# Kernel optimization log

Hardware: AMD Instinct MI355X
Metric: run time of the kernel (lower is better)

## Reference

```python
import jax, jax.numpy as jnp
import numpy as np

B, L = 256, 256
TAU = 0.01


def setup_inputs() -> dict:
    key = jax.random.key(0)
    k1, k2, k3, k4 = jax.random.split(key, 4)
    x = jax.random.normal(k1, (B, L, B), dtype=jnp.float32)
    target = jax.random.normal(k2, (B, L, B), dtype=jnp.float32)
    mask = jnp.ones((B, L), dtype=jnp.int32)  # prefix-valid mask per query; all clips valid
    query_labels = jax.random.randint(k3, (B,), 0, B, dtype=jnp.int64)
    label_mat = jax.random.randint(k4, (B, B), 0, 2, dtype=jnp.int32)  # label_dict[i] -> row i
    return {"x": x, "target": target, "mask": mask, "query_labels": query_labels, "label_mat": label_mat}


def reference(x, target, mask, query_labels, label_mat):
    # x, target: [B, L, B] (batch, clips, queries); mask: [B(queries), L]
    xs = jax.nn.softmax(x, axis=1)
    ts = jax.nn.softmax(target, axis=1)
    m = (mask > 0).astype(xs.dtype)  # [i(query), l]
    # mask target clips per query i (equivalent to the original's :m prefix slice
    # because mask is a contiguous prefix of valid clips)
    tsm = ts * m.T[None, :, :]  # [c, l, i]
    # sim[i, b, c] = sum_l xs[b, l, i] * ts[c, l, i] * m[i, l]  (per-query B x B matmul)
    sim = jnp.einsum('bli,cli->ibc', xs, tsm)
    logits = sim / TAU
    # original computes -log(exp(n_ji)/sum_c exp(n_jc)) == -log_softmax over c, picked at class i
    logp = jax.nn.log_softmax(logits, axis=-1)  # [i, j, c]
    per = jnp.diagonal(logp, axis1=0, axis2=2)  # per[j, i] = logp[i, j, i]
    loss = -(label_mat.astype(xs.dtype).T * per).sum() / x.shape[0]
    return loss
```

## Files before the change

### kernel.cpp

```cpp
#include <hip/hip_runtime.h>
#include <hip/hip_bf16.h>

#define NB 256
#define NL 256
#define SCALE 100.0f

typedef __attribute__((ext_vector_type(4))) unsigned int u32x4;
typedef __attribute__((ext_vector_type(8))) __bf16 bfrag8;
typedef __attribute__((ext_vector_type(4))) float f32x4;

union BU { bfrag8 f; u32x4 u; };

static __device__ __forceinline__ unsigned int pack2bf(float a, float b) {
  union { float f; unsigned int u; } ua, ub;
  ua.f = a; ub.f = b;
  unsigned int ra = (ua.u + 0x7FFFu + ((ua.u >> 16) & 1u)) >> 16;
  unsigned int rb = (ub.u + 0x7FFFu + ((ub.u >> 16) & 1u)) & 0xFFFF0000u;
  return ra | rb;
}

__global__ __launch_bounds__(1024, 2) void exp_t(
    const float* __restrict__ x, const float* __restrict__ tgt,
    unsigned int* __restrict__ xsT, unsigned int* __restrict__ tsT)
{
  const int b = blockIdx.x;
  const bool is_t = (blockIdx.y != 0);
  const int tid = threadIdx.x;
  const int i = tid & 255;
  const int h = tid >> 8;
  const float* src = (is_t ? tgt : x) + (size_t)b * (NL * NB) + i;
  unsigned int* dstb = (is_t ? tsT : xsT);

  __shared__ __align__(16) unsigned char stg[256 * 128];

  const int r0 = tid >> 3;
  const int c  = tid & 7;

  for (int lc = 0; lc < 4; ++lc) {
    float v[16];
    #pragma unroll
    for (int k = 0; k < 16; ++k)
      v[k] = __expf(src[(size_t)(lc * 64 + h * 16 + k) * NB]);
    u32x4 p0, p1;
    p0.x = pack2bf(v[0], v[1]);   p0.y = pack2bf(v[2], v[3]);
    p0.z = pack2bf(v[4], v[5]);   p0.w = pack2bf(v[6], v[7]);
    p1.x = pack2bf(v[8], v[9]);   p1.y = pack2bf(v[10], v[11]);
    p1.z = pack2bf(v[12], v[13]); p1.w = pack2bf(v[14], v[15]);
    *reinterpret_cast<u32x4*>(&stg[i * 128 + (((h * 2 + 0) ^ (i & 7)) << 4)]) = p0;
    *reinterpret_cast<u32x4*>(&stg[i * 128 + (((h * 2 + 1) ^ (i & 7)) << 4)]) = p1;
    __syncthreads();
    u32x4 q0 = *reinterpret_cast<const u32x4*>(&stg[r0 * 128 + ((c ^ (r0 & 7)) << 4)]);
    u32x4 q1 = *reinterpret_cast<const u32x4*>(&stg[(r0 + 128) * 128 + ((c ^ (r0 & 7)) << 4)]);
    *reinterpret_cast<u32x4*>(dstb + ((size_t)r0 * 256 + b) * 128 + lc * 32 + c * 4) = q0;
    *reinterpret_cast<u32x4*>(dstb + ((size_t)(r0 + 128) * 256 + b) * 128 + lc * 32 + c * 4) = q1;
    __syncthreads();
  }
}

__global__ __launch_bounds__(256, 2) void gemm_lse(
    const unsigned short* __restrict__ xsT,
    const unsigned short* __restrict__ tsT,
    const int* __restrict__ mask,
    const int* __restrict__ label_mat,
    float* __restrict__ out)
{
  const int n  = blockIdx.x;
  const int g  = n & 7;
  const int q  = n >> 3;
  const int i  = ((q >> 2) << 3) + g;
  const int jt = q & 3;
  const int t  = threadIdx.x;
  const int w  = t >> 6;
  const int lane = t & 63;

  __shared__ __align__(16) unsigned char As[64 * 128];
  __shared__ __align__(16) unsigned char Bs[256 * 128];
  __shared__ __align__(16) unsigned short s_mask[NL];
  __shared__ float s_rmax[4][64];
  __shared__ float s_rsum[4][64];
  __shared__ float s_diag[64];

  const unsigned short* Ag = xsT + ((size_t)i * NB + jt * 64) * NL;
  const unsigned short* Bg = tsT + (size_t)i * NB * NL;

  const int srow = t >> 3;
  const int sch  = t & 7;

  s_mask[t] = (mask[i * NL + t] > 0) ? (unsigned short)0xFFFFu : (unsigned short)0u;

  BU onesbu;
  onesbu.u = u32x4{0x3F803F80u, 0x3F803F80u, 0x3F803F80u, 0x3F803F80u};
  const bfrag8 ones = onesbu.f;

  f32x4 acc[4][4], acc_as[4], acc_bs[4];
  #pragma unroll
  for (int a = 0; a < 4; ++a) {
    acc_as[a] = f32x4{0.f, 0.f, 0.f, 0.f};
    acc_bs[a] = f32x4{0.f, 0.f, 0.f, 0.f};
    #pragma unroll
    for (int cc = 0; cc < 4; ++cc) acc[a][cc] = f32x4{0.f, 0.f, 0.f, 0.f};
  }

  u32x4 areg[2], breg[8];

  #pragma unroll
  for (int r = 0; r < 2; ++r)
    areg[r] = *reinterpret_cast<const u32x4*>(Ag + (size_t)(srow + r * 32) * NL + sch * 8);
  #pragma unroll
  for (int r = 0; r < 8; ++r)
    breg[r] = *reinterpret_cast<const u32x4*>(Bg + (size_t)(srow + r * 32) * NL + sch * 8);

  __syncthreads();

  #pragma unroll
  for (int kc = 0; kc < 4; ++kc) {
    #pragma unroll
    for (int r = 0; r < 2; ++r) {
      int row = srow + r * 32;
      *reinterpret_cast<u32x4*>(&As[row * 128 + ((sch ^ (row & 7)) << 4)]) = areg[r];
    }
    #pragma unroll
    for (int r = 0; r < 8; ++r) {
      int row = srow + r * 32;
      *reinterpret_cast<u32x4*>(&Bs[row * 128 + ((sch ^ (row & 7)) << 4)]) = breg[r];
    }
    __syncthreads();
    if (kc < 3) {
      const int kofs = (kc + 1) * 64;
      #pragma unroll
      for (int r = 0; r < 2; ++r)
        areg[r] = *reinterpret_cast<const u32x4*>(Ag + (size_t)(srow + r * 32) * NL + kofs + sch * 8);
      #pragma unroll
      for (int r = 0; r < 8; ++r)
        breg[r] = *reinterpret_cast<const u32x4*>(Bg + (size_t)(srow + r * 32) * NL + kofs + sch * 8);
    }
    #pragma unroll
    for (int kk = 0; kk < 2; ++kk) {
      const int co = kk * 4 + (lane >> 4);
      bfrag8 af[4], bfr[4];
      #pragma unroll
      for (int jf = 0; jf < 4; ++jf) {
        int row = jf * 16 + (lane & 15);
        af[jf] = *reinterpret_cast<const bfrag8*>(&As[row * 128 + ((co ^ (row & 7)) << 4)]);
      }
      #pragma unroll
      for (int cf = 0; cf < 4; ++cf) {
        int row = w * 64 + cf * 16 + (lane & 15);
        bfr[cf] = *reinterpret_cast<const bfrag8*>(&Bs[row * 128 + ((co ^ (row & 7)) << 4)]);
      }
      u32x4 mk = *reinterpret_cast<const u32x4*>(
          &s_mask[kc * 64 + kk * 32 + ((lane >> 4) << 3)]);
      #pragma unroll
      for (int jf = 0; jf < 4; ++jf) {
        BU am; am.f = af[jf]; am.u &= mk;
        #pragma unroll
        for (int cf = 0; cf < 4; ++cf)
          acc[jf][cf] = __builtin_amdgcn_mfma_f32_16x16x32_bf16(
              am.f, bfr[cf], acc[jf][cf], 0, 0, 0);
        acc_as[jf] = __builtin_amdgcn_mfma_f32_16x16x32_bf16(
            af[jf], ones, acc_as[jf], 0, 0, 0);
      }
      #pragma unroll
      for (int cf = 0; cf < 4; ++cf)
        acc_bs[cf] = __builtin_amdgcn_mfma_f32_16x16x32_bf16(
            ones, bfr[cf], acc_bs[cf], 0, 0, 0);
    }
    __syncthreads();
  }

  float ixv[4][4];
  #pragma unroll
  for (int jf = 0; jf < 4; ++jf)
    #pragma unroll
    for (int reg = 0; reg < 4; ++reg)
      ixv[jf][reg] = __builtin_amdgcn_rcpf(acc_as[jf][reg]) * SCALE;
  float itv[4];
  #pragma unroll
  for (int cf = 0; cf < 4; ++cf)
    itv[cf] = __builtin_amdgcn_rcpf(acc_bs[cf][0]);
  #pragma unroll
  for (int jf = 0; jf < 4; ++jf)
    #pragma unroll
    for (int cf = 0; cf < 4; ++cf)
      #pragma unroll
      for (int reg = 0; reg < 4; ++reg)
        acc[jf][cf][reg] *= ixv[jf][reg] * itv[cf];

  const int rg = (lane >> 4) << 2;

  #pragma unroll
  for (int jf = 0; jf < 4; ++jf) {
    #pragma unroll
    for (int reg = 0; reg < 4; ++reg) {
      float m = fmaxf(fmaxf(acc[jf][0][reg], acc[jf][1][reg]),
                      fmaxf(acc[jf][2][reg], acc[jf][3][reg]));
      #pragma unroll
      for (int off = 1; off < 16; off <<= 1) m = fmaxf(m, __shfl_xor(m, off, 64));
      if ((lane & 15) == 0) s_rmax[w][jf * 16 + rg + reg] = m;
    }
  }
  if (w == (i >> 6) && (lane & 15) == (i & 15)) {
    const int cfd = (i >> 4) & 3;
    #pragma unroll
    for (int jf = 0; jf < 4; ++jf) {
      #pragma unroll
      for (int reg = 0; reg < 4; ++reg) {
        float v = acc[jf][0][reg];
        #pragma unroll
        for (int cf = 1; cf < 4; ++cf)
          v = (cfd == cf) ? acc[jf][cf][reg] : v;
        s_diag[jf * 16 + rg + reg] = v;
      }
    }
  }
  __syncthreads();

  #pragma unroll
  for (int jf = 0; jf < 4; ++jf) {
    #pragma unroll
    for (int reg = 0; reg < 4; ++reg) {
      int row = jf * 16 + rg + reg;
      float gm = fmaxf(fmaxf(s_rmax[0][row], s_rmax[1][row]),
                       fmaxf(s_rmax[2][row], s_rmax[3][row]));
      float sE = 0.f;
      #pragma unroll
      for (int cf = 0; cf < 4; ++cf) sE += __expf(acc[jf][cf][reg] - gm);
      #pragma unroll
      for (int off = 1; off < 16; off <<= 1) sE += __shfl_xor(sE, off, 64);
      if ((lane & 15) == 0) s_rsum[w][row] = sE;
    }
  }
  __syncthreads();

  float contrib = 0.f;
  if (t < 64) {
    const int row = t;
    float gm = fmaxf(fmaxf(s_rmax[0][row], s_rmax[1][row]),
                     fmaxf(s_rmax[2][row], s_rmax[3][row]));
    float tot = s_rsum[0][row] + s_rsum[1][row] + s_rsum[2][row] + s_rsum[3][row];
    float lse = __logf(tot) + gm;
    float lbl = (float)label_mat[i * NB + jt * 64 + row];
    contrib = lbl * (s_diag[row] - lse);
  }
  #pragma unroll
  for (int off = 32; off >= 1; off >>= 1) contrib += __shfl_down(contrib, off, 64);
  if (t == 0) atomicAdd(out, contrib * (-1.0f / 256.0f));
}

extern "C" void kernel_launch(void* const* d_in, const int* in_sizes, int n_in,
                              void* d_out, int out_size, void* d_ws, size_t ws_size,
                              hipStream_t stream) {
  const float* x   = (const float*)d_in[0];
  const float* tgt = (const float*)d_in[1];
  const int* mask  = (const int*)d_in[2];
  const int* label_mat = (const int*)d_in[4];
  float* out = (float*)d_out;

  unsigned int* xsT = (unsigned int*)d_ws;
  unsigned int* tsT = xsT + (size_t)NB * NB * NL / 2;

  hipMemsetAsync(out, 0, sizeof(float), stream);
  exp_t<<<dim3(NB, 2), 1024, 0, stream>>>(x, tgt, xsT, tsT);
  gemm_lse<<<dim3(1024), 256, 0, stream>>>((const unsigned short*)xsT,
                                           (const unsigned short*)tsT,
                                           mask, label_mat, out);
}
```

Measured before the change: 75.98 us.

## Vectorize exp-transpose loads, double-buffer staging, and deepen GEMM global prefetch

The exp/transpose kernel now reads inputs as float4 along the query dimension instead of strided scalars. It stages through two LDS buffers with an extra XOR swizzle, which lets it drop the trailing barrier per chunk. The GEMM kernel keeps two register sets of global loads in flight, prefetching two k-chunks ahead, so global latency overlaps with MFMA work. In exchange, LDS use in the first kernel doubles and the GEMM holds more live registers, which may hurt occupancy.

Result: no change. 74.91 us (-1.4%).

```diff
diff --git a/kernel.cpp b/kernel.cpp
--- a/kernel.cpp
+++ b/kernel.cpp
@@ -26,34 +26,40 @@
   const int b = blockIdx.x;
   const bool is_t = (blockIdx.y != 0);
   const int tid = threadIdx.x;
-  const int i = tid & 255;
-  const int h = tid >> 8;
-  const float* src = (is_t ? tgt : x) + (size_t)b * (NL * NB) + i;
+  const int i4 = tid & 63;
+  const int g  = tid >> 6;
+  const f32x4* src4 = reinterpret_cast<const f32x4*>(
+      (is_t ? tgt : x) + (size_t)b * (NL * NB));
   unsigned int* dstb = (is_t ? tsT : xsT);
 
-  __shared__ __align__(16) unsigned char stg[256 * 128];
+  __shared__ __align__(16) unsigned char stg[2][256 * 128];
 
   const int r0 = tid >> 3;
   const int c  = tid & 7;
 
+  #pragma unroll
   for (int lc = 0; lc < 4; ++lc) {
-    float v[16];
-    #pragma unroll
-    for (int k = 0; k < 16; ++k)
-      v[k] = __expf(src[(size_t)(lc * 64 + h * 16 + k) * NB]);
-    u32x4 p0, p1;
-    p0.x = pack2bf(v[0], v[1]);   p0.y = pack2bf(v[2], v[3]);
-    p0.z = pack2bf(v[4], v[5]);   p0.w = pack2bf(v[6], v[7]);
-    p1.x = pack2bf(v[8], v[9]);   p1.y = pack2bf(v[10], v[11]);
-    p1.z = pack2bf(v[12], v[13]); p1.w = pack2bf(v[14], v[15]);
-    *reinterpret_cast<u32x4*>(&stg[i * 128 + (((h * 2 + 0) ^ (i & 7)) << 4)]) = p0;
-    *reinterpret_cast<u32x4*>(&stg[i * 128 + (((h * 2 + 1) ^ (i & 7)) << 4)]) = p1;
+    unsigned char* sb = stg[lc & 1];
+    f32x4 r[4];
+    #pragma unroll
+    for (int k = 0; k < 4; ++k)
+      r[k] = src4[(size_t)(lc * 64 + g * 4 + k) * 64 + i4];
+    #pragma unroll
+    for (int ii = 0; ii < 4; ++ii) {
+      const int row = i4 * 4 + ii;
+      unsigned int lo = pack2bf(__expf(r[0][ii]), __expf(r[1][ii]));
+      unsigned int hi = pack2bf(__expf(r[2][ii]), __expf(r[3][ii]));
+      const int ch = (g >> 1) ^ (row & 7) ^ ((row >> 3) & 7);
+      unsigned int* p = reinterpret_cast<unsigned int*>(
+          &sb[row * 128 + (ch << 4) + (g & 1) * 8]);
+      p[0] = lo; p[1] = hi;
+    }
     __syncthreads();
-    u32x4 q0 = *reinterpret_cast<const u32x4*>(&stg[r0 * 128 + ((c ^ (r0 & 7)) << 4)]);
-    u32x4 q1 = *reinterpret_cast<const u32x4*>(&stg[(r0 + 128) * 128 + ((c ^ (r0 & 7)) << 4)]);
+    const int ch0 = c ^ (r0 & 7) ^ ((r0 >> 3) & 7);
+    u32x4 q0 = *reinterpret_cast<const u32x4*>(&sb[r0 * 128 + (ch0 << 4)]);
+    u32x4 q1 = *reinterpret_cast<const u32x4*>(&sb[(r0 + 128) * 128 + (ch0 << 4)]);
     *reinterpret_cast<u32x4*>(dstb + ((size_t)r0 * 256 + b) * 128 + lc * 32 + c * 4) = q0;
     *reinterpret_cast<u32x4*>(dstb + ((size_t)(r0 + 128) * 256 + b) * 128 + lc * 32 + c * 4) = q1;
-    __syncthreads();
   }
 }
 
@@ -101,39 +107,32 @@
     for (int cc = 0; cc < 4; ++cc) acc[a][cc] = f32x4{0.f, 0.f, 0.f, 0.f};
   }
 
-  u32x4 areg[2], breg[8];
-
-  #pragma unroll
-  for (int r = 0; r < 2; ++r)
-    areg[r] = *reinterpret_cast<const u32x4*>(Ag + (size_t)(srow + r * 32) * NL + sch * 8);
-  #pragma unroll
-  for (int r = 0; r < 8; ++r)
-    breg[r] = *reinterpret_cast<const u32x4*>(Bg + (size_t)(srow + r * 32) * NL + sch * 8);
-
-  __syncthreads();
-
-  #pragma unroll
-  for (int kc = 0; kc < 4; ++kc) {
+  u32x4 a0[2], b0[8], a1[2], b1[8];
+
+  auto load_set = [&](u32x4 (&ar)[2], u32x4 (&br)[8], int kc) {
+    const int kofs = kc * 64;
+    #pragma unroll
+    for (int r = 0; r < 2; ++r)
+      ar[r] = *reinterpret_cast<const u32x4*>(
+          Ag + (size_t)(srow + r * 32) * NL + kofs + sch * 8);
+    #pragma unroll
+    for (int r = 0; r < 8; ++r)
+      br[r] = *reinterpret_cast<const u32x4*>(
+          Bg + (size_t)(srow + r * 32) * NL + kofs + sch * 8);
+  };
+  auto store_set = [&](u32x4 (&ar)[2], u32x4 (&br)[8]) {
     #pragma unroll
     for (int r = 0; r < 2; ++r) {
       int row = srow + r * 32;
-      *reinterpret_cast<u32x4*>(&As[row * 128 + ((sch ^ (row & 7)) << 4)]) = areg[r];
+      *reinterpret_cast<u32x4*>(&As[row * 128 + ((sch ^ (row & 7)) << 4)]) = ar[r];
     }
     #pragma unroll
     for (int r = 0; r < 8; ++r) {
       int row = srow + r * 32;
-      *reinterpret_cast<u32x4*>(&Bs[row * 128 + ((sch ^ (row & 7)) << 4)]) = breg[r];
-    }
-    __syncthreads();
-    if (kc < 3) {
-      const int kofs = (kc + 1) * 64;
-      #pragma unroll
-      for (int r = 0; r < 2; ++r)
-        areg[r] = *reinterpret_cast<const u32x4*>(Ag + (size_t)(srow + r * 32) * NL + kofs + sch * 8);
-      #pragma unroll
-      for (int r = 0; r < 8; ++r)
-        breg[r] = *reinterpret_cast<const u32x4*>(Bg + (size_t)(srow + r * 32) * NL + kofs + sch * 8);
-    }
+      *reinterpret_cast<u32x4*>(&Bs[row * 128 + ((sch ^ (row & 7)) << 4)]) = br[r];
+    }
+  };
+  auto mfma_phase = [&](int kc) {
     #pragma unroll
     for (int kk = 0; kk < 2; ++kk) {
       const int co = kk * 4 + (lane >> 4);
@@ -141,12 +140,14 @@
       #pragma unroll
       for (int jf = 0; jf < 4; ++jf) {
         int row = jf * 16 + (lane & 15);
-        af[jf] = *reinterpret_cast<const bfrag8*>(&As[row * 128 + ((co ^ (row & 7)) << 4)]);
+        af[jf] = *reinterpret_cast<const bfrag8*>(
+            &As[row * 128 + ((co ^ (row & 7)) << 4)]);
       }
       #pragma unroll
       for (int cf = 0; cf < 4; ++cf) {
         int row = w * 64 + cf * 16 + (lane & 15);
-        bfr[cf] = *reinterpret_cast<const bfrag8*>(&Bs[row * 128 + ((co ^ (row & 7)) << 4)]);
+        bfr[cf] = *reinterpret_cast<const bfrag8*>(
+            &Bs[row * 128 + ((co ^ (row & 7)) << 4)]);
       }
       u32x4 mk = *reinterpret_cast<const u32x4*>(
           &s_mask[kc * 64 + kk * 32 + ((lane >> 4) << 3)]);
@@ -165,8 +166,27 @@
         acc_bs[cf] = __builtin_amdgcn_mfma_f32_16x16x32_bf16(
             ones, bfr[cf], acc_bs[cf], 0, 0, 0);
     }
-    __syncthreads();
-  }
+  };
+
+  load_set(a0, b0, 0);
+  load_set(a1, b1, 1);
+  store_set(a0, b0);
+  __syncthreads();
+  load_set(a0, b0, 2);
+  mfma_phase(0);
+  __syncthreads();
+  store_set(a1, b1);
+  __syncthreads();
+  load_set(a1, b1, 3);
+  mfma_phase(1);
+  __syncthreads();
+  store_set(a0, b0);
+  __syncthreads();
+  mfma_phase(2);
+  __syncthreads();
+  store_set(a1, b1);
+  __syncthreads();
+  mfma_phase(3);
 
   float ixv[4][4];
   #pragma unroll
```

## Stage GEMM tiles with direct global-to-LDS loads and double-buffered B

Applied to the files above, without the earlier changes.

The GEMM kernel stops staging tiles through registers. It issues global_load_lds 16-byte loads that write straight into LDS with the XOR swizzle applied at the source address, and double-buffers the B tile so the next K chunk loads while MFMAs run. The A fragments for both k-substeps are read up front so As can be refilled early. The exp_t output layout changes from [r][b] to [b][r] to match the new addressing, and a swizzle index bug in the second staging read is fixed. The trade-offs are hand-placed waitcnt and barrier calls that carry correctness risk, and more LDS per block, which may lower occupancy.

Measured after the change: 77.23 us. Within noise of the previous version (+1.6%).

```diff
diff --git a/kernel.cpp b/kernel.cpp
--- a/kernel.cpp
+++ b/kernel.cpp
@@ -17,6 +17,12 @@
   unsigned int ra = (ua.u + 0x7FFFu + ((ua.u >> 16) & 1u)) >> 16;
   unsigned int rb = (ub.u + 0x7FFFu + ((ub.u >> 16) & 1u)) & 0xFFFF0000u;
   return ra | rb;
+}
+
+static __device__ __forceinline__ void gld_lds16(const void* g, void* l) {
+  __builtin_amdgcn_global_load_lds(
+      (const __attribute__((address_space(1))) unsigned int*)g,
+      (__attribute__((address_space(3))) unsigned int*)l, 16, 0, 0);
 }
 
 __global__ __launch_bounds__(1024, 2) void exp_t(
@@ -50,9 +56,9 @@
     *reinterpret_cast<u32x4*>(&stg[i * 128 + (((h * 2 + 1) ^ (i & 7)) << 4)]) = p1;
     __syncthreads();
     u32x4 q0 = *reinterpret_cast<const u32x4*>(&stg[r0 * 128 + ((c ^ (r0 & 7)) << 4)]);
-    u32x4 q1 = *reinterpret_cast<const u32x4*>(&stg[(r0 + 128) * 128 + ((c ^ (r0 & 7)) << 4)]);
-    *reinterpret_cast<u32x4*>(dstb + ((size_t)r0 * 256 + b) * 128 + lc * 32 + c * 4) = q0;
-    *reinterpret_cast<u32x4*>(dstb + ((size_t)(r0 + 128) * 256 + b) * 128 + lc * 32 + c * 4) = q1;
+    u32x4 q1 = *reinterpret_cast<const u32x4*>(&stg[(r0 + 128) * 128 + ((c ^ ((r0 + 128) & 7)) << 4)]);
+    *reinterpret_cast<u32x4*>(dstb + ((size_t)b * 256 + r0) * 128 + lc * 32 + c * 4) = q0;
+    *reinterpret_cast<u32x4*>(dstb + ((size_t)b * 256 + r0 + 128) * 128 + lc * 32 + c * 4) = q1;
     __syncthreads();
   }
 }
@@ -74,15 +80,12 @@
   const int lane = t & 63;
 
   __shared__ __align__(16) unsigned char As[64 * 128];
-  __shared__ __align__(16) unsigned char Bs[256 * 128];
+  __shared__ __align__(16) unsigned char Bs[2][256 * 128];
   __shared__ __align__(16) unsigned short s_mask[NL];
   __shared__ float s_rmax[4][64];
   __shared__ float s_rsum[4][64];
   __shared__ float s_diag[64];
 
-  const unsigned short* Ag = xsT + ((size_t)i * NB + jt * 64) * NL;
-  const unsigned short* Bg = tsT + (size_t)i * NB * NL;
-
   const int srow = t >> 3;
   const int sch  = t & 7;
 
@@ -101,71 +104,77 @@
     for (int cc = 0; cc < 4; ++cc) acc[a][cc] = f32x4{0.f, 0.f, 0.f, 0.f};
   }
 
-  u32x4 areg[2], breg[8];
-
-  #pragma unroll
-  for (int r = 0; r < 2; ++r)
-    areg[r] = *reinterpret_cast<const u32x4*>(Ag + (size_t)(srow + r * 32) * NL + sch * 8);
-  #pragma unroll
-  for (int r = 0; r < 8; ++r)
-    breg[r] = *reinterpret_cast<const u32x4*>(Bg + (size_t)(srow + r * 32) * NL + sch * 8);
-
-  __syncthreads();
-
-  #pragma unroll
-  for (int kc = 0; kc < 4; ++kc) {
-    #pragma unroll
-    for (int r = 0; r < 2; ++r) {
-      int row = srow + r * 32;
-      *reinterpret_cast<u32x4*>(&As[row * 128 + ((sch ^ (row & 7)) << 4)]) = areg[r];
-    }
+  auto stage_B = [&](int buf, int kc2) {
+    const int kofs = kc2 * 64;
     #pragma unroll
     for (int r = 0; r < 8; ++r) {
       int row = srow + r * 32;
-      *reinterpret_cast<u32x4*>(&Bs[row * 128 + ((sch ^ (row & 7)) << 4)]) = breg[r];
-    }
-    __syncthreads();
-    if (kc < 3) {
-      const int kofs = (kc + 1) * 64;
-      #pragma unroll
-      for (int r = 0; r < 2; ++r)
-        areg[r] = *reinterpret_cast<const u32x4*>(Ag + (size_t)(srow + r * 32) * NL + kofs + sch * 8);
-      #pragma unroll
-      for (int r = 0; r < 8; ++r)
-        breg[r] = *reinterpret_cast<const u32x4*>(Bg + (size_t)(srow + r * 32) * NL + kofs + sch * 8);
-    }
+      int schp = sch ^ (row & 7);
+      gld_lds16(tsT + ((size_t)row * 256 + i) * 256 + kofs + schp * 8,
+                &Bs[buf][w * 1024 + r * 4096]);
+    }
+  };
+  auto stage_A = [&](int kc2) {
+    const int kofs = kc2 * 64;
+    #pragma unroll
+    for (int r = 0; r < 2; ++r) {
+      int arow = srow + r * 32;
+      int schp = sch ^ (arow & 7);
+      gld_lds16(xsT + ((size_t)(jt * 64 + arow) * 256 + i) * 256 + kofs + schp * 8,
+                &As[w * 1024 + r * 4096]);
+    }
+  };
+
+  stage_B(0, 0);
+  stage_A(0);
+  __syncthreads();
+
+  #pragma unroll
+  for (int kc = 0; kc < 4; ++kc) {
+    const int cur = kc & 1;
+    if (kc < 3) stage_B(cur ^ 1, kc + 1);
+    bfrag8 af0[4], af1[4];
+    #pragma unroll
+    for (int jf = 0; jf < 4; ++jf) {
+      int row = jf * 16 + (lane & 15);
+      int co0 = 0 * 4 + (lane >> 4), co1 = 1 * 4 + (lane >> 4);
+      af0[jf] = *reinterpret_cast<const bfrag8*>(&As[row * 128 + ((co0 ^ (row & 7)) << 4)]);
+      af1[jf] = *reinterpret_cast<const bfrag8*>(&As[row * 128 + ((co1 ^ (row & 7)) << 4)]);
+    }
+    asm volatile("s_waitcnt lgkmcnt(0)" ::: "memory");
+    __builtin_amdgcn_sched_barrier(0);
+    __builtin_amdgcn_s_barrier();
+    if (kc < 3) stage_A(kc + 1);
     #pragma unroll
     for (int kk = 0; kk < 2; ++kk) {
       const int co = kk * 4 + (lane >> 4);
-      bfrag8 af[4], bfr[4];
-      #pragma unroll
-      for (int jf = 0; jf < 4; ++jf) {
-        int row = jf * 16 + (lane & 15);
-        af[jf] = *reinterpret_cast<const bfrag8*>(&As[row * 128 + ((co ^ (row & 7)) << 4)]);
-      }
+      bfrag8 bfr[4];
       #pragma unroll
       for (int cf = 0; cf < 4; ++cf) {
         int row = w * 64 + cf * 16 + (lane & 15);
-        bfr[cf] = *reinterpret_cast<const bfrag8*>(&Bs[row * 128 + ((co ^ (row & 7)) << 4)]);
+        bfr[cf] = *reinterpret_cast<const bfrag8*>(
+            &Bs[cur][row * 128 + ((co ^ (row & 7)) << 4)]);
       }
       u32x4 mk = *reinterpret_cast<const u32x4*>(
           &s_mask[kc * 64 + kk * 32 + ((lane >> 4) << 3)]);
       #pragma unroll
       for (int jf = 0; jf < 4; ++jf) {
-        BU am; am.f = af[jf]; am.u &= mk;
+        BU am; am.f = (kk == 0) ? af0[jf] : af1[jf]; am.u &= mk;
         #pragma unroll
         for (int cf = 0; cf < 4; ++cf)
           acc[jf][cf] = __builtin_amdgcn_mfma_f32_16x16x32_bf16(
               am.f, bfr[cf], acc[jf][cf], 0, 0, 0);
         acc_as[jf] = __builtin_amdgcn_mfma_f32_16x16x32_bf16(
-            af[jf], ones, acc_as[jf], 0, 0, 0);
+            (kk == 0) ? af0[jf] : af1[jf], ones, acc_as[jf], 0, 0, 0);
       }
       #pragma unroll
       for (int cf = 0; cf < 4; ++cf)
         acc_bs[cf] = __builtin_amdgcn_mfma_f32_16x16x32_bf16(
             ones, bfr[cf], acc_bs[cf], 0, 0, 0);
     }
-    __syncthreads();
+    asm volatile("s_waitcnt vmcnt(0)" ::: "memory");
+    __builtin_amdgcn_sched_barrier(0);
+    __builtin_amdgcn_s_barrier();
   }
 
   float ixv[4][4];
```

## Enlarge GEMM tile to 128 rows and transpose intermediate layout to batch-major

Applied to the files above, without the earlier changes.

The GEMM kernel now processes 128 query-row tiles with 512 threads (8 waves in a 2x4 arrangement) instead of 64-row tiles with 256 threads. This halves the number of blocks and halves the redundant loading of the shared B operand per query index. The intermediate bf16 softmax buffers switch from query-major to batch-major layout, which changes the exp/transposition kernel's store pattern and makes the GEMM loads strided across batch rows. Fewer blocks may lower occupancy and latency hiding.

Result: no change. 76.86 us (+1.2%).

```diff
diff --git a/kernel.cpp b/kernel.cpp
--- a/kernel.cpp
+++ b/kernel.cpp
@@ -50,14 +50,14 @@
     *reinterpret_cast<u32x4*>(&stg[i * 128 + (((h * 2 + 1) ^ (i & 7)) << 4)]) = p1;
     __syncthreads();
     u32x4 q0 = *reinterpret_cast<const u32x4*>(&stg[r0 * 128 + ((c ^ (r0 & 7)) << 4)]);
-    u32x4 q1 = *reinterpret_cast<const u32x4*>(&stg[(r0 + 128) * 128 + ((c ^ (r0 & 7)) << 4)]);
-    *reinterpret_cast<u32x4*>(dstb + ((size_t)r0 * 256 + b) * 128 + lc * 32 + c * 4) = q0;
-    *reinterpret_cast<u32x4*>(dstb + ((size_t)(r0 + 128) * 256 + b) * 128 + lc * 32 + c * 4) = q1;
+    u32x4 q1 = *reinterpret_cast<const u32x4*>(&stg[(r0 + 128) * 128 + ((c ^ ((r0 + 128) & 7)) << 4)]);
+    *reinterpret_cast<u32x4*>(dstb + ((size_t)b * 256 + r0) * 128 + lc * 32 + c * 4) = q0;
+    *reinterpret_cast<u32x4*>(dstb + ((size_t)b * 256 + r0 + 128) * 128 + lc * 32 + c * 4) = q1;
     __syncthreads();
   }
 }
 
-__global__ __launch_bounds__(256, 2) void gemm_lse(
+__global__ __launch_bounds__(512, 2) void gemm_lse(
     const unsigned short* __restrict__ xsT,
     const unsigned short* __restrict__ tsT,
     const int* __restrict__ mask,
@@ -67,26 +67,23 @@
   const int n  = blockIdx.x;
   const int g  = n & 7;
   const int q  = n >> 3;
-  const int i  = ((q >> 2) << 3) + g;
-  const int jt = q & 3;
+  const int i  = ((q >> 1) << 3) + g;
+  const int jt = q & 1;
   const int t  = threadIdx.x;
   const int w  = t >> 6;
   const int lane = t & 63;
-
-  __shared__ __align__(16) unsigned char As[64 * 128];
+  const int wr = w >> 2;
+  const int wc = w & 3;
+
+  __shared__ __align__(16) unsigned char As[128 * 128];
   __shared__ __align__(16) unsigned char Bs[256 * 128];
   __shared__ __align__(16) unsigned short s_mask[NL];
-  __shared__ float s_rmax[4][64];
-  __shared__ float s_rsum[4][64];
-  __shared__ float s_diag[64];
-
-  const unsigned short* Ag = xsT + ((size_t)i * NB + jt * 64) * NL;
-  const unsigned short* Bg = tsT + (size_t)i * NB * NL;
-
-  const int srow = t >> 3;
-  const int sch  = t & 7;
-
-  s_mask[t] = (mask[i * NL + t] > 0) ? (unsigned short)0xFFFFu : (unsigned short)0u;
+  __shared__ float s_rmax[4][128];
+  __shared__ float s_rsum[4][128];
+  __shared__ float s_diag[128];
+
+  if (t < 256)
+    s_mask[t] = (mask[i * NL + t] > 0) ? (unsigned short)0xFFFFu : (unsigned short)0u;
 
   BU onesbu;
   onesbu.u = u32x4{0x3F803F80u, 0x3F803F80u, 0x3F803F80u, 0x3F803F80u};
@@ -101,52 +98,61 @@
     for (int cc = 0; cc < 4; ++cc) acc[a][cc] = f32x4{0.f, 0.f, 0.f, 0.f};
   }
 
-  u32x4 areg[2], breg[8];
-
-  #pragma unroll
-  for (int r = 0; r < 2; ++r)
-    areg[r] = *reinterpret_cast<const u32x4*>(Ag + (size_t)(srow + r * 32) * NL + sch * 8);
-  #pragma unroll
-  for (int r = 0; r < 8; ++r)
-    breg[r] = *reinterpret_cast<const u32x4*>(Bg + (size_t)(srow + r * 32) * NL + sch * 8);
-
-  __syncthreads();
-
+  u32x4 areg[2], breg[4];
+
+  auto load_chunk = [&](int kc) {
+    const int kofs = kc * 64;
+    #pragma unroll
+    for (int r = 0; r < 2; ++r) {
+      int u = t + r * 512;
+      int row = u >> 3, ch = u & 7;
+      areg[r] = *reinterpret_cast<const u32x4*>(
+          xsT + ((size_t)(jt * 128 + row) * 256 + i) * 256 + kofs + ch * 8);
+    }
+    #pragma unroll
+    for (int r = 0; r < 4; ++r) {
+      int u = t + r * 512;
+      int row = u >> 3, ch = u & 7;
+      breg[r] = *reinterpret_cast<const u32x4*>(
+          tsT + ((size_t)row * 256 + i) * 256 + kofs + ch * 8);
+    }
+  };
+  auto store_chunk = [&]() {
+    #pragma unroll
+    for (int r = 0; r < 2; ++r) {
+      int u = t + r * 512;
+      int row = u >> 3, ch = u & 7;
+      *reinterpret_cast<u32x4*>(&As[row * 128 + ((ch ^ (row & 7)) << 4)]) = areg[r];
+    }
+    #pragma unroll
+    for (int r = 0; r < 4; ++r) {
+      int u = t + r * 512;
+      int row = u >> 3, ch = u & 7;
+      *reinterpret_cast<u32x4*>(&Bs[row * 128 + ((ch ^ (row & 7)) << 4)]) = breg[r];
+    }
+  };
+
+  load_chunk(0);
   #pragma unroll
   for (int kc = 0; kc < 4; ++kc) {
-    #pragma unroll
-    for (int r = 0; r < 2; ++r) {
-      int row = srow + r * 32;
-      *reinterpret_cast<u32x4*>(&As[row * 128 + ((sch ^ (row & 7)) << 4)]) = areg[r];
-    }
-    #pragma unroll
-    for (int r = 0; r < 8; ++r) {
-      int row = srow + r * 32;
-      *reinterpret_cast<u32x4*>(&Bs[row * 128 + ((sch ^ (row & 7)) << 4)]) = breg[r];
-    }
+    store_chunk();
     __syncthreads();
-    if (kc < 3) {
-      const int kofs = (kc + 1) * 64;
-      #pragma unroll
-      for (int r = 0; r < 2; ++r)
-        areg[r] = *reinterpret_cast<const u32x4*>(Ag + (size_t)(srow + r * 32) * NL + kofs + sch * 8);
-      #pragma unroll
-      for (int r = 0; r < 8; ++r)
-        breg[r] = *reinterpret_cast<const u32x4*>(Bg + (size_t)(srow + r * 32) * NL + kofs + sch * 8);
-    }
+    if (kc < 3) load_chunk(kc + 1);
     #pragma unroll
     for (int kk = 0; kk < 2; ++kk) {
       const int co = kk * 4 + (lane >> 4);
       bfrag8 af[4], bfr[4];
       #pragma unroll
       for (int jf = 0; jf < 4; ++jf) {
-        int row = jf * 16 + (lane & 15);
-        af[jf] = *reinterpret_cast<const bfrag8*>(&As[row * 128 + ((co ^ (row & 7)) << 4)]);
+        int row = wr * 64 + jf * 16 + (lane & 15);
+        af[jf] = *reinterpret_cast<const bfrag8*>(
+            &As[row * 128 + ((co ^ (row & 7)) << 4)]);
       }
       #pragma unroll
       for (int cf = 0; cf < 4; ++cf) {
-        int row = w * 64 + cf * 16 + (lane & 15);
-        bfr[cf] = *reinterpret_cast<const bfrag8*>(&Bs[row * 128 + ((co ^ (row & 7)) << 4)]);
+        int row = wc * 64 + cf * 16 + (lane & 15);
+        bfr[cf] = *reinterpret_cast<const bfrag8*>(
+            &Bs[row * 128 + ((co ^ (row & 7)) << 4)]);
       }
       u32x4 mk = *reinterpret_cast<const u32x4*>(
           &s_mask[kc * 64 + kk * 32 + ((lane >> 4) << 3)]);
@@ -165,7 +171,7 @@
         acc_bs[cf] = __builtin_amdgcn_mfma_f32_16x16x32_bf16(
             ones, bfr[cf], acc_bs[cf], 0, 0, 0);
     }
-    __syncthreads();
+    if (kc < 3) __syncthreads();
   }
 
   float ixv[4][4];
@@ -196,10 +202,10 @@
                       fmaxf(acc[jf][2][reg], acc[jf][3][reg]));
       #pragma unroll
       for (int off = 1; off < 16; off <<= 1) m = fmaxf(m, __shfl_xor(m, off, 64));
-      if ((lane & 15) == 0) s_rmax[w][jf * 16 + rg + reg] = m;
-    }
-  }
-  if (w == (i >> 6) && (lane & 15) == (i & 15)) {
+      if ((lane & 15) == 0) s_rmax[wc][wr * 64 + jf * 16 + rg + reg] = m;
+    }
+  }
+  if (wc == (i >> 6) && (lane & 15) == (i & 15)) {
     const int cfd = (i >> 4) & 3;
     #pragma unroll
     for (int jf = 0; jf < 4; ++jf) {
@@ -209,7 +215,7 @@
         #pragma unroll
         for (int cf = 1; cf < 4; ++cf)
           v = (cfd == cf) ? acc[jf][cf][reg] : v;
-        s_diag[jf * 16 + rg + reg] = v;
+        s_diag[wr * 64 + jf * 16 + rg + reg] = v;
       }
     }
   }
@@ -219,7 +225,7 @@
   for (int jf = 0; jf < 4; ++jf) {
     #pragma unroll
     for (int reg = 0; reg < 4; ++reg) {
-      int row = jf * 16 + rg + reg;
+      int row = wr * 64 + jf * 16 + rg + reg;
       float gm = fmaxf(fmaxf(s_rmax[0][row], s_rmax[1][row]),
                        fmaxf(s_rmax[2][row], s_rmax[3][row]));
       float sE = 0.f;
@@ -227,24 +233,24 @@
       for (int cf = 0; cf < 4; ++cf) sE += __expf(acc[jf][cf][reg] - gm);
       #pragma unroll
       for (int off = 1; off < 16; off <<= 1) sE += __shfl_xor(sE, off, 64);
-      if ((lane & 15) == 0) s_rsum[w][row] = sE;
+      if ((lane & 15) == 0) s_rsum[wc][row] = sE;
     }
   }
   __syncthreads();
 
   float contrib = 0.f;
-  if (t < 64) {
+  if (t < 128) {
     const int row = t;
     float gm = fmaxf(fmaxf(s_rmax[0][row], s_rmax[1][row]),
                      fmaxf(s_rmax[2][row], s_rmax[3][row]));
     float tot = s_rsum[0][row] + s_rsum[1][row] + s_rsum[2][row] + s_rsum[3][row];
     float lse = __logf(tot) + gm;
-    float lbl = (float)label_mat[i * NB + jt * 64 + row];
+    float lbl = (float)label_mat[i * NB + jt * 128 + row];
     contrib = lbl * (s_diag[row] - lse);
   }
   #pragma unroll
   for (int off = 32; off >= 1; off >>= 1) contrib += __shfl_down(contrib, off, 64);
-  if (t == 0) atomicAdd(out, contrib * (-1.0f / 256.0f));
+  if (lane == 0 && w < 2) atomicAdd(out, contrib * (-1.0f / 256.0f));
 }
 
 extern "C" void kernel_launch(void* const* d_in, const int* in_sizes, int n_in,
@@ -261,7 +267,7 @@
 
   hipMemsetAsync(out, 0, sizeof(float), stream);
   exp_t<<<dim3(NB, 2), 1024, 0, stream>>>(x, tgt, xsT, tsT);
-  gemm_lse<<<dim3(1024), 256, 0, stream>>>((const unsigned short*)xsT,
-                                           (const unsigned short*)tsT,
-                                           mask, label_mat, out);
-}
+  gemm_lse<<<dim3(512), 512, 0, stream>>>((const unsigned short*)xsT,
+                                          (const unsigned short*)tsT,
+                                          mask, label_mat, out);
+}
```
